# Kernel optimization log

Measured on AMD Instinct MI355X. Metric: run time of the kernel, lower is better.

The kernel has to match this reference:

```python
import jax, jax.numpy as jnp
import numpy as np

B, S, D, H = 8, 256, 16, 256
NH, DH, L = 8, H // 8, 3
H2, H4, FF = H // 2, H // 4, 2 * H


def _ln(x, g, b, eps=1e-5):
    m = jnp.mean(x, axis=-1, keepdims=True)
    v = jnp.var(x, axis=-1, keepdims=True)
    return (x - m) / jnp.sqrt(v + eps) * g + b


def setup_inputs() -> dict:
    key = jax.random.key(0)
    ks = iter(jax.random.split(key, 32))
    w = lambda *sh: jax.random.normal(next(ks), sh, jnp.float32) * 0.05
    inp = {
        'parts': jax.random.normal(next(ks), (B, S, D), jnp.float32),
        'target_sequence': jax.random.randint(next(ks), (B, S), 0, S),
        # part encoder
        'W_pe1': w(H2, D), 'b_pe1': jnp.zeros((H2,)),
        'W_pe2': w(H2, H2), 'b_pe2': jnp.zeros((H2,)),
        'pos_emb': w(S, H4),
        # transformer encoder (3 layers, stacked)
        'Wqkv': w(L, 3 * H, H), 'bqkv': jnp.zeros((L, 3 * H)),
        'Wo': w(L, H, H), 'bo': jnp.zeros((L, H)),
        'ln1_g': jnp.ones((L, H)), 'ln1_b': jnp.zeros((L, H)),
        'W1f': w(L, FF, H), 'b1f': jnp.zeros((L, FF)),
        'W2f': w(L, H, FF), 'b2f': jnp.zeros((L, H)),
        'ln2_g': jnp.ones((L, H)), 'ln2_b': jnp.zeros((L, H)),
        # LSTM decoder
        'Wih': w(4 * H, H), 'Whh': w(4 * H, H),
        'bih': jnp.zeros((4 * H,)), 'bhh': jnp.zeros((4 * H,)),
        # pointer
        'Wp': w(H, H), 'bp': jnp.zeros((H,)), 'v_ptr': w(H),
    }
    return inp


def reference(parts, target_sequence, W_pe1, b_pe1, W_pe2, b_pe2, pos_emb,
              Wqkv, bqkv, Wo, bo, ln1_g, ln1_b, W1f, b1f, W2f, b2f, ln2_g, ln2_b,
              Wih, Whh, bih, bhh, Wp, bp, v_ptr):
    Bk, Sk = parts.shape[:2]
    # ---- encode_inputs (dropout inactive in eval) ----
    pe = jax.nn.relu(parts @ W_pe1.T + b_pe1) @ W_pe2.T + b_pe2          # [B,S,H/2]
    pos = jnp.broadcast_to(pos_emb[None, :Sk], (Bk, Sk, H4))              # [B,S,H/4]
    pad = jnp.zeros((Bk, Sk, H - H2 - H4), parts.dtype)
    x = jnp.concatenate([pe, pos, pad], axis=-1)                          # [B,S,H]
    scale = 1.0 / np.sqrt(DH)
    for l in range(L):  # post-norm transformer encoder layers
        qkv = x @ Wqkv[l].T + bqkv[l]
        q, k, v = jnp.split(qkv, 3, axis=-1)
        q = q.reshape(Bk, Sk, NH, DH)
        k = k.reshape(Bk, Sk, NH, DH)
        v = v.reshape(Bk, Sk, NH, DH)
        att = jax.nn.softmax(jnp.einsum('bqhd,bkhd->bhqk', q, k) * scale, axis=-1)
        o = jnp.einsum('bhqk,bkhd->bqhd', att, v).reshape(Bk, Sk, H)
        o = o @ Wo[l].T + bo[l]
        x = _ln(x + o, ln1_g[l], ln1_b[l])
        f = jax.nn.relu(x @ W1f[l].T + b1f[l]) @ W2f[l].T + b2f[l]
        x = _ln(x + f, ln2_g[l], ln2_b[l])
    enc = x                                                               # [B,S,H]
    # ---- teacher-forced LSTM decode (teacher_forcing_ratio=1.0) ----
    gathered = jnp.take_along_axis(enc, target_sequence[:, :, None], axis=1)  # [B,T,H]
    dec_in = jnp.concatenate([jnp.zeros((Bk, 1, H), enc.dtype), gathered[:, :-1]], 1)
    dec_in = dec_in.transpose(1, 0, 2)                                    # [T,B,H]

    def step(carry, xt):
        h, c = carry
        g = xt @ Wih.T + bih + h @ Whh.T + bhh
        i, f, gg, o = jnp.split(g, 4, axis=-1)
        c = jax.nn.sigmoid(f) * c + jax.nn.sigmoid(i) * jnp.tanh(gg)
        h = jax.nn.sigmoid(o) * jnp.tanh(c)
        return (h, c), h

    h0 = jnp.zeros((Bk, H), enc.dtype)
    _, dec_out = jax.lax.scan(step, (h0, h0), dec_in)
    dec_out = dec_out.transpose(1, 0, 2)                                  # [B,T,H]
    # ---- pointer logits: v . tanh(Wp d_t + Wp e_i), batched over (t,i) ----
    pd = dec_out @ Wp.T + bp                                              # [B,T,H]
    pen = enc @ Wp.T + bp                                                 # [B,S,H]
    logits = jnp.tanh(pd[:, :, None, :] + pen[:, None, :, :]) @ v_ptr     # [B,T,S]
    return logits
```

## Files before the change

kernel.cpp:

```cpp
#include <hip/hip_runtime.h>
#include <cstdint>
#include <cstddef>

typedef _Float16 h2 __attribute__((ext_vector_type(2)));
typedef short bf16x8 __attribute__((ext_vector_type(8)));
typedef float f32x4 __attribute__((ext_vector_type(4)));

__device__ __forceinline__ float sigf(float x) { return 1.0f / (1.0f + __expf(-x)); }
__device__ __forceinline__ float tanhfast(float x) {
  float e = __expf(-2.0f * fabsf(x));
  float t = (1.0f - e) / (1.0f + e);
  return copysignf(t, x);
}
__device__ __forceinline__ h2 cvt2(float a, float b) {
  h2 r; r.x = (_Float16)a; r.y = (_Float16)b; return r;
}
__device__ __forceinline__ h2 bch2(unsigned int u) { return __builtin_bit_cast(h2, u); }
__device__ __forceinline__ unsigned int bcu(h2 v) { return __builtin_bit_cast(unsigned int, v); }
__device__ __forceinline__ unsigned short f2bf(float f) {
  unsigned int u = __float_as_uint(f);
  u = (u + 0x7fffu + ((u >> 16) & 1u)) >> 16;
  return (unsigned short)u;
}

__device__ __forceinline__ float fdot2f(h2 a, h2 b, float c) {
#if __has_builtin(__builtin_amdgcn_fdot2)
  return __builtin_amdgcn_fdot2(a, b, c, false);
#else
  return fmaf((float)a.x, (float)b.x, fmaf((float)a.y, (float)b.y, c));
#endif
}

__global__ void convert_bf(const float* __restrict__ src, ushort* __restrict__ dst, int n) {
  int i = blockIdx.x * 256 + threadIdx.x;
  if (i < n) dst[i] = f2bf(src[i]);
}

__global__ void part_encoder(const float* __restrict__ parts, const float* __restrict__ Wpe1,
                             const float* __restrict__ bpe1, const float* __restrict__ Wpe2,
                             const float* __restrict__ bpe2, const float* __restrict__ pos,
                             float* __restrict__ x, ushort* __restrict__ xb) {
  __shared__ float prow[16];
  __shared__ float pe1[128];
  int row = blockIdx.x;
  int s = row & 255;
  int tid = threadIdx.x;
  if (tid < 16) prow[tid] = parts[row * 16 + tid];
  __syncthreads();
  float a = bpe1[tid];
#pragma unroll
  for (int k = 0; k < 16; ++k) a = fmaf(prow[k], Wpe1[tid * 16 + k], a);
  pe1[tid] = fmaxf(a, 0.0f);
  __syncthreads();
  float a2 = bpe2[tid];
  for (int k = 0; k < 128; ++k) a2 = fmaf(pe1[k], Wpe2[tid * 128 + k], a2);
  x[(size_t)row * 256 + tid] = a2;
  xb[(size_t)row * 256 + tid] = f2bf(a2);
  if (tid < 64) {
    float p = pos[s * 64 + tid];
    x[(size_t)row * 256 + 128 + tid] = p;
    xb[(size_t)row * 256 + 128 + tid] = f2bf(p);
    x[(size_t)row * 256 + 192 + tid] = 0.0f;
    xb[(size_t)row * 256 + 192 + tid] = 0;
  }
}

template <int ACT, int OUTBF>
__global__ __launch_bounds__(256) void gemm_bf16(
    const ushort* __restrict__ A, const ushort* __restrict__ Wt,
    const float* __restrict__ bias1, const float* __restrict__ bias2,
    void* __restrict__ Cout, int N, int K) {
  int wid = threadIdx.x >> 6;
  int lane = threadIdx.x & 63;
  int m0 = blockIdx.y * 64 + wid * 16;
  int n0 = blockIdx.x * 64;
  int r15 = lane & 15;
  int kg = lane >> 4;
  f32x4 acc0 = {0.f, 0.f, 0.f, 0.f}, acc1 = acc0, acc2 = acc0, acc3 = acc0;
  const ushort* arow = A + (size_t)(m0 + r15) * K + kg * 8;
  const ushort* w0 = Wt + (size_t)(n0 + r15) * K + kg * 8;
  const ushort* w1 = w0 + (size_t)16 * K;
  const ushort* w2 = w0 + (size_t)32 * K;
  const ushort* w3 = w0 + (size_t)48 * K;
  for (int k0 = 0; k0 < K; k0 += 32) {
    bf16x8 af = *(const bf16x8*)(arow + k0);
    bf16x8 b0 = *(const bf16x8*)(w0 + k0);
    bf16x8 b1 = *(const bf16x8*)(w1 + k0);
    bf16x8 b2 = *(const bf16x8*)(w2 + k0);
    bf16x8 b3 = *(const bf16x8*)(w3 + k0);
    acc0 = __builtin_amdgcn_mfma_f32_16x16x32_bf16(af, b0, acc0, 0, 0, 0);
    acc1 = __builtin_amdgcn_mfma_f32_16x16x32_bf16(af, b1, acc1, 0, 0, 0);
    acc2 = __builtin_amdgcn_mfma_f32_16x16x32_bf16(af, b2, acc2, 0, 0, 0);
    acc3 = __builtin_amdgcn_mfma_f32_16x16x32_bf16(af, b3, acc3, 0, 0, 0);
  }
#pragma unroll
  for (int nn = 0; nn < 4; ++nn) {
    f32x4 a = (nn == 0) ? acc0 : (nn == 1) ? acc1 : (nn == 2) ? acc2 : acc3;
    int n = n0 + nn * 16 + r15;
    float bsum = bias1[n] + (bias2 ? bias2[n] : 0.0f);
#pragma unroll
    for (int r = 0; r < 4; ++r) {
      int m = m0 + kg * 4 + r;
      float v = a[r] + bsum;
      if (ACT == 1) v = fmaxf(v, 0.0f);
      if (OUTBF == 1)
        ((ushort*)Cout)[(size_t)m * N + n] = f2bf(v);
      else
        ((float*)Cout)[(size_t)m * N + n] = v;
    }
  }
}

__global__ void attn_kernel(const float* __restrict__ qkv, ushort* __restrict__ attout) {
  extern __shared__ float sm[];
  float* kl = sm;
  float* ql = sm + 256 * 33;
  float* sc = sm + 256 * 33 + 32 * 33;
  int qt = blockIdx.x, h = blockIdx.y, b = blockIdx.z;
  int tid = threadIdx.x;
  {
    int j = tid;
    const float* src = qkv + (size_t)(b * 256 + j) * 768 + 256 + h * 32;
#pragma unroll
    for (int d = 0; d < 32; d += 4) {
      float4 v = *(const float4*)(src + d);
      kl[j * 33 + d] = v.x; kl[j * 33 + d + 1] = v.y; kl[j * 33 + d + 2] = v.z; kl[j * 33 + d + 3] = v.w;
    }
  }
  {
    int i = tid >> 3, d4 = (tid & 7) * 4;
    const float* src = qkv + (size_t)(b * 256 + qt * 32 + i) * 768 + h * 32;
    float4 v = *(const float4*)(src + d4);
    ql[i * 33 + d4] = v.x; ql[i * 33 + d4 + 1] = v.y; ql[i * 33 + d4 + 2] = v.z; ql[i * 33 + d4 + 3] = v.w;
  }
  __syncthreads();
  int i = tid >> 3, c = tid & 7;
  const float scale = 0.17677669529663687f;
  float sv[32];
  float mx = -1e30f;
  for (int jj = 0; jj < 32; ++jj) {
    int j = jj * 8 + c;
    float s = 0.0f;
#pragma unroll
    for (int d = 0; d < 32; ++d) s = fmaf(ql[i * 33 + d], kl[j * 33 + d], s);
    s *= scale;
    sv[jj] = s;
    mx = fmaxf(mx, s);
  }
  mx = fmaxf(mx, __shfl_xor(mx, 1));
  mx = fmaxf(mx, __shfl_xor(mx, 2));
  mx = fmaxf(mx, __shfl_xor(mx, 4));
  float sum = 0.0f;
  for (int jj = 0; jj < 32; ++jj) {
    float p = __expf(sv[jj] - mx);
    sc[i * 257 + jj * 8 + c] = p;
    sum += p;
  }
  sum += __shfl_xor(sum, 1);
  sum += __shfl_xor(sum, 2);
  sum += __shfl_xor(sum, 4);
  float inv = 1.0f / sum;
  __syncthreads();
  float a0 = 0, a1 = 0, a2 = 0, a3 = 0;
  int d0 = c * 4;
  const float* vbase = qkv + 512 + h * 32 + d0;
  for (int j = 0; j < 256; ++j) {
    float p = sc[i * 257 + j];
    float4 v = *(const float4*)(vbase + (size_t)(b * 256 + j) * 768);
    a0 = fmaf(p, v.x, a0); a1 = fmaf(p, v.y, a1); a2 = fmaf(p, v.z, a2); a3 = fmaf(p, v.w, a3);
  }
  int orow = b * 256 + qt * 32 + i;
  ushort4 o4;
  o4.x = f2bf(a0 * inv); o4.y = f2bf(a1 * inv); o4.z = f2bf(a2 * inv); o4.w = f2bf(a3 * inv);
  *(ushort4*)&attout[(size_t)orow * 256 + h * 32 + d0] = o4;
}

__global__ void ln_residual(float* __restrict__ x, const float* __restrict__ o,
                            const float* __restrict__ g, const float* __restrict__ bt,
                            ushort* __restrict__ xb) {
  int row = blockIdx.x, tid = threadIdx.x;
  float e = x[(size_t)row * 256 + tid] + o[(size_t)row * 256 + tid];
  float s = e, q = e * e;
#pragma unroll
  for (int off = 32; off >= 1; off >>= 1) {
    s += __shfl_xor(s, off);
    q += __shfl_xor(q, off);
  }
  __shared__ float ps[4], pq[4];
  int wid = tid >> 6, lane = tid & 63;
  if (lane == 0) { ps[wid] = s; pq[wid] = q; }
  __syncthreads();
  float St = ps[0] + ps[1] + ps[2] + ps[3];
  float Qt = pq[0] + pq[1] + pq[2] + pq[3];
  float mean = St * (1.0f / 256.0f);
  float var = Qt * (1.0f / 256.0f) - mean * mean;
  float y = (e - mean) * rsqrtf(var + 1e-5f) * g[tid] + bt[tid];
  x[(size_t)row * 256 + tid] = y;
  xb[(size_t)row * 256 + tid] = f2bf(y);
}

__global__ void gather_dec_in(const ushort* __restrict__ encb, const int* __restrict__ ts,
                              ushort* __restrict__ dec_in) {
  int bx = blockIdx.x;
  int t = bx >> 3, b = bx & 7;
  int tid = threadIdx.x;
  ushort4 v = {0, 0, 0, 0};
  if (t > 0) {
    int sidx = ts[b * 256 + t - 1];
    v = *(const ushort4*)&encb[((size_t)(b * 256 + sidx)) * 256 + tid * 4];
  }
  *(ushort4*)&dec_in[(size_t)bx * 256 + tid * 4] = v;
}

__global__ __attribute__((amdgpu_flat_work_group_size(512, 512), amdgpu_waves_per_eu(1, 1)))
void lstm_scan(const float* __restrict__ Xw, const float* __restrict__ Whh,
               ushort* __restrict__ dec_out) {
  extern __shared__ char smem[];
  uint4* wlds = (uint4*)smem;
  h2* hbuf = (h2*)(smem + 131072);
  int b = blockIdx.x;
  int t0 = threadIdx.x;
  int u = t0 >> 1, p = t0 & 1;
  int rA = u + 256 * p;
  int rB = u + 512 + 256 * p;

  h2 w0[96], w1[96];
  {
    const float4* sA = (const float4*)(Whh + (size_t)rA * 256);
    const float4* sB = (const float4*)(Whh + (size_t)rB * 256);
#pragma unroll
    for (int k = 0; k < 48; ++k) {
      float4 v = sA[k];
      w0[2 * k] = cvt2(v.x, v.y);
      w0[2 * k + 1] = cvt2(v.z, v.w);
    }
#pragma unroll
    for (int k = 0; k < 48; ++k) {
      float4 v = sB[k];
      w1[2 * k] = cvt2(v.x, v.y);
      w1[2 * k + 1] = cvt2(v.z, v.w);
    }
#pragma unroll
    for (int qc = 0; qc < 8; ++qc) {
      float4 vA0 = sA[48 + 2 * qc], vA1 = sA[48 + 2 * qc + 1];
      float4 vB0 = sB[48 + 2 * qc], vB1 = sB[48 + 2 * qc + 1];
      uint4 uA, uB;
      uA.x = bcu(cvt2(vA0.x, vA0.y)); uA.y = bcu(cvt2(vA0.z, vA0.w));
      uA.z = bcu(cvt2(vA1.x, vA1.y)); uA.w = bcu(cvt2(vA1.z, vA1.w));
      uB.x = bcu(cvt2(vB0.x, vB0.y)); uB.y = bcu(cvt2(vB0.z, vB0.w));
      uB.z = bcu(cvt2(vB1.x, vB1.y)); uB.w = bcu(cvt2(vB1.z, vB1.w));
      wlds[qc * 1024 + rA] = uA;
      wlds[qc * 1024 + rB] = uB;
    }
  }
  if (t0 < 128) ((uint4*)hbuf)[t0 & 63] = make_uint4(0, 0, 0, 0);
  float c = 0.0f;
  float xnA = Xw[(size_t)b * 1024 + rA];
  float xnB = Xw[(size_t)b * 1024 + rB];
  __syncthreads();

  for (int t = 0; t < 256; ++t) {
    float xwA = xnA, xwB = xnB;
    if (t < 255) {
      const float* xp = Xw + (size_t)((t + 1) * 8 + b) * 1024;
      xnA = xp[rA]; xnB = xp[rB];
    }
    const uint4* hb = (const uint4*)(hbuf + (size_t)(t & 1) * 128);
    float a0 = 0.0f, a1 = 0.0f;
#pragma unroll
    for (int q = 0; q < 24; ++q) {
      uint4 hv = hb[q];
      h2 hx = bch2(hv.x), hy = bch2(hv.y), hz = bch2(hv.z), hw = bch2(hv.w);
      a0 = fdot2f(w0[4 * q], hx, a0); a0 = fdot2f(w0[4 * q + 1], hy, a0);
      a0 = fdot2f(w0[4 * q + 2], hz, a0); a0 = fdot2f(w0[4 * q + 3], hw, a0);
      a1 = fdot2f(w1[4 * q], hx, a1); a1 = fdot2f(w1[4 * q + 1], hy, a1);
      a1 = fdot2f(w1[4 * q + 2], hz, a1); a1 = fdot2f(w1[4 * q + 3], hw, a1);
    }
#pragma unroll
    for (int qc = 0; qc < 8; ++qc) {
      uint4 hv = hb[24 + qc];
      h2 hx = bch2(hv.x), hy = bch2(hv.y), hz = bch2(hv.z), hw = bch2(hv.w);
      uint4 uA = wlds[qc * 1024 + rA];
      uint4 uB = wlds[qc * 1024 + rB];
      a0 = fdot2f(bch2(uA.x), hx, a0); a0 = fdot2f(bch2(uA.y), hy, a0);
      a0 = fdot2f(bch2(uA.z), hz, a0); a0 = fdot2f(bch2(uA.w), hw, a0);
      a1 = fdot2f(bch2(uB.x), hx, a1); a1 = fdot2f(bch2(uB.y), hy, a1);
      a1 = fdot2f(bch2(uB.z), hz, a1); a1 = fdot2f(bch2(uB.w), hw, a1);
    }
    a0 += xwA;
    a1 += xwB;
    float ev = sigf(a0) * tanhfast(a1);
    float ep = __shfl_xor(ev, 1);
    if (p == 1) {
      c = sigf(a0) * c + ep;
      float hv_ = sigf(a1) * tanhfast(c);
      ((_Float16*)(hbuf + (size_t)((t + 1) & 1) * 128))[u] = (_Float16)hv_;
      dec_out[((size_t)(b * 256 + t)) * 256 + u] = f2bf(hv_);
    }
    __syncthreads();
  }
}

__global__ void transpose_pen(const float* __restrict__ pen, float* __restrict__ penT) {
  int bx = blockIdx.x;
  int b = bx >> 8, h = bx & 255;
  int i = threadIdx.x;
  penT[(size_t)bx * 256 + i] = pen[((size_t)(b * 256 + i)) * 256 + h];
}

__global__ void pointer_kernel(const float* __restrict__ pd, const float* __restrict__ penT,
                               const float* __restrict__ vptr, float* __restrict__ out) {
  __shared__ float pdr[256];
  __shared__ float vl[256];
  int bx = blockIdx.x;
  int b = bx >> 8;
  int tid = threadIdx.x;
  pdr[tid] = pd[(size_t)bx * 256 + tid];
  vl[tid] = vptr[tid];
  __syncthreads();
  const float* pT = penT + (size_t)b * 256 * 256;
  float acc = 0.0f;
  for (int h = 0; h < 256; ++h) {
    acc = fmaf(vl[h], tanhfast(pdr[h] + pT[(size_t)h * 256 + tid]), acc);
  }
  out[(size_t)bx * 256 + tid] = acc;
}

extern "C" void kernel_launch(void* const* d_in, const int* in_sizes, int n_in,
                              void* d_out, int out_size, void* d_ws, size_t ws_size,
                              hipStream_t stream) {
  const float* parts = (const float*)d_in[0];
  const int* ts = (const int*)d_in[1];
  const float* Wpe1 = (const float*)d_in[2];
  const float* bpe1 = (const float*)d_in[3];
  const float* Wpe2 = (const float*)d_in[4];
  const float* bpe2 = (const float*)d_in[5];
  const float* pos = (const float*)d_in[6];
  const float* Wqkv = (const float*)d_in[7];
  const float* bqkv = (const float*)d_in[8];
  const float* Wo = (const float*)d_in[9];
  const float* bo = (const float*)d_in[10];
  const float* ln1g = (const float*)d_in[11];
  const float* ln1b = (const float*)d_in[12];
  const float* W1f = (const float*)d_in[13];
  const float* b1f = (const float*)d_in[14];
  const float* W2f = (const float*)d_in[15];
  const float* b2f = (const float*)d_in[16];
  const float* ln2g = (const float*)d_in[17];
  const float* ln2b = (const float*)d_in[18];
  const float* Wih = (const float*)d_in[19];
  const float* Whh = (const float*)d_in[20];
  const float* bih = (const float*)d_in[21];
  const float* bhh = (const float*)d_in[22];
  const float* Wp = (const float*)d_in[23];
  const float* bp = (const float*)d_in[24];
  const float* vptr = (const float*)d_in[25];
  float* out = (float*)d_out;

  float* W = (float*)d_ws;
  float* xbuf = W;
  ushort* xbf = (ushort*)(W + 524288);
  float* SCR = W + 786432;
  float* qkvb = SCR;
  float* obuf = SCR + 1572864;
  float* Xw = SCR;
  float* pdb = SCR;
  float* penb = SCR + 524288;
  float* penTb = SCR + 1048576;
  ushort* attbf = (ushort*)(W + 2883584);
  ushort* ffbf = (ushort*)(W + 3145728);
  ushort* dec_inbf = (ushort*)(W + 3145728);
  ushort* dec_outbf = (ushort*)(W + 3407872);
  ushort* wqkvbf = (ushort*)(W + 3670016);
  ushort* wobf   = (ushort*)(W + 3964928);
  ushort* w1fbf  = (ushort*)(W + 4063232);
  ushort* w2fbf  = (ushort*)(W + 4259840);
  ushort* wihbf  = (ushort*)(W + 4456448);
  ushort* wpbf   = (ushort*)(W + 4587520);

  const int attnLDS = (256 * 33 + 32 * 33 + 32 * 257) * 4;
  const int scanLDS = 131072 + 1024;
  hipFuncSetAttribute((const void*)attn_kernel, hipFuncAttributeMaxDynamicSharedMemorySize, attnLDS);
  hipFuncSetAttribute((const void*)lstm_scan, hipFuncAttributeMaxDynamicSharedMemorySize, scanLDS);

  convert_bf<<<(589824 + 255) / 256, 256, 0, stream>>>(Wqkv, wqkvbf, 589824);
  convert_bf<<<(196608 + 255) / 256, 256, 0, stream>>>(Wo, wobf, 196608);
  convert_bf<<<(393216 + 255) / 256, 256, 0, stream>>>(W1f, w1fbf, 393216);
  convert_bf<<<(393216 + 255) / 256, 256, 0, stream>>>(W2f, w2fbf, 393216);
  convert_bf<<<(262144 + 255) / 256, 256, 0, stream>>>(Wih, wihbf, 262144);
  convert_bf<<<(65536 + 255) / 256, 256, 0, stream>>>(Wp, wpbf, 65536);

  part_encoder<<<2048, 128, 0, stream>>>(parts, Wpe1, bpe1, Wpe2, bpe2, pos, xbuf, xbf);
  for (int l = 0; l < 3; ++l) {
    gemm_bf16<0, 0><<<dim3(12, 32), 256, 0, stream>>>(xbf, wqkvbf + (size_t)l * 196608,
                                                      bqkv + l * 768, nullptr, qkvb, 768, 256);
    attn_kernel<<<dim3(8, 8, 8), 256, attnLDS, stream>>>(qkvb, attbf);
    gemm_bf16<0, 0><<<dim3(4, 32), 256, 0, stream>>>(attbf, wobf + (size_t)l * 65536,
                                                     bo + l * 256, nullptr, obuf, 256, 256);
    ln_residual<<<2048, 256, 0, stream>>>(xbuf, obuf, ln1g + l * 256, ln1b + l * 256, xbf);
    gemm_bf16<1, 1><<<dim3(8, 32), 256, 0, stream>>>(xbf, w1fbf + (size_t)l * 131072,
                                                     b1f + l * 512, nullptr, ffbf, 512, 256);
    gemm_bf16<0, 0><<<dim3(4, 32), 256, 0, stream>>>(ffbf, w2fbf + (size_t)l * 131072,
                                                     b2f + l * 256, nullptr, obuf, 256, 512);
    ln_residual<<<2048, 256, 0, stream>>>(xbuf, obuf, ln2g + l * 256, ln2b + l * 256, xbf);
  }
  gather_dec_in<<<2048, 64, 0, stream>>>(xbf, ts, dec_inbf);
  gemm_bf16<0, 0><<<dim3(16, 32), 256, 0, stream>>>(dec_inbf, wihbf, bih, bhh, Xw, 1024, 256);
  lstm_scan<<<8, 512, scanLDS, stream>>>(Xw, Whh, dec_outbf);
  gemm_bf16<0, 0><<<dim3(4, 32), 256, 0, stream>>>(dec_outbf, wpbf, bp, nullptr, pdb, 256, 256);
  gemm_bf16<0, 0><<<dim3(4, 32), 256, 0, stream>>>(xbf, wpbf, bp, nullptr, penb, 256, 256);
  transpose_pen<<<2048, 256, 0, stream>>>(penb, penTb);
  pointer_kernel<<<2048, 256, 0, stream>>>(pdb, penTb, vptr, out);
}
```

Measured before the change: 863.2 us.

## Quantize LSTM recurrence to int8 sdot4, merge weight conversions, fuse pen transpose

After: 849.1 us. About the same (-1.6%).

```diff
diff --git a/kernel.cpp b/kernel.cpp
--- a/kernel.cpp
+++ b/kernel.cpp
@@ -5,6 +5,12 @@
 typedef _Float16 h2 __attribute__((ext_vector_type(2)));
 typedef short bf16x8 __attribute__((ext_vector_type(8)));
 typedef float f32x4 __attribute__((ext_vector_type(4)));
+
+#if __has_builtin(__builtin_amdgcn_sdot4)
+#define HAVE_SDOT4 1
+#else
+#define HAVE_SDOT4 0
+#endif
 
 __device__ __forceinline__ float sigf(float x) { return 1.0f / (1.0f + __expf(-x)); }
 __device__ __forceinline__ float tanhfast(float x) {
@@ -31,9 +37,24 @@
 #endif
 }
 
-__global__ void convert_bf(const float* __restrict__ src, ushort* __restrict__ dst, int n) {
+__global__ void convert_all(const float* __restrict__ s0, ushort* __restrict__ d0,
+                            const float* __restrict__ s1, ushort* __restrict__ d1,
+                            const float* __restrict__ s2, ushort* __restrict__ d2,
+                            const float* __restrict__ s3, ushort* __restrict__ d3,
+                            const float* __restrict__ s4, ushort* __restrict__ d4,
+                            const float* __restrict__ s5, ushort* __restrict__ d5) {
   int i = blockIdx.x * 256 + threadIdx.x;
-  if (i < n) dst[i] = f2bf(src[i]);
+  if (i < 589824) { d0[i] = f2bf(s0[i]); return; }
+  i -= 589824;
+  if (i < 196608) { d1[i] = f2bf(s1[i]); return; }
+  i -= 196608;
+  if (i < 393216) { d2[i] = f2bf(s2[i]); return; }
+  i -= 393216;
+  if (i < 393216) { d3[i] = f2bf(s3[i]); return; }
+  i -= 393216;
+  if (i < 262144) { d4[i] = f2bf(s4[i]); return; }
+  i -= 262144;
+  if (i < 65536) d5[i] = f2bf(s5[i]);
 }
 
 __global__ void part_encoder(const float* __restrict__ parts, const float* __restrict__ Wpe1,
@@ -65,7 +86,7 @@
   }
 }
 
-template <int ACT, int OUTBF>
+template <int ACT, int OUT>
 __global__ __launch_bounds__(256) void gemm_bf16(
     const ushort* __restrict__ A, const ushort* __restrict__ Wt,
     const float* __restrict__ bias1, const float* __restrict__ bias2,
@@ -98,15 +119,22 @@
     f32x4 a = (nn == 0) ? acc0 : (nn == 1) ? acc1 : (nn == 2) ? acc2 : acc3;
     int n = n0 + nn * 16 + r15;
     float bsum = bias1[n] + (bias2 ? bias2[n] : 0.0f);
-#pragma unroll
-    for (int r = 0; r < 4; ++r) {
-      int m = m0 + kg * 4 + r;
-      float v = a[r] + bsum;
-      if (ACT == 1) v = fmaxf(v, 0.0f);
-      if (OUTBF == 1)
-        ((ushort*)Cout)[(size_t)m * N + n] = f2bf(v);
-      else
-        ((float*)Cout)[(size_t)m * N + n] = v;
+    if (OUT == 3) {
+      int b = m0 >> 8;
+      int mloc = (m0 & 255) + kg * 4;
+      float4 o4 = {a[0] + bsum, a[1] + bsum, a[2] + bsum, a[3] + bsum};
+      *(float4*)&((float*)Cout)[((size_t)(b * 256 + n)) * 256 + mloc] = o4;
+    } else {
+#pragma unroll
+      for (int r = 0; r < 4; ++r) {
+        int m = m0 + kg * 4 + r;
+        float v = a[r] + bsum;
+        if (ACT == 1) v = fmaxf(v, 0.0f);
+        if (OUT == 1)
+          ((ushort*)Cout)[(size_t)m * N + n] = f2bf(v);
+        else
+          ((float*)Cout)[(size_t)m * N + n] = v;
+      }
     }
   }
 }
@@ -212,9 +240,114 @@
   *(ushort4*)&dec_in[(size_t)bx * 256 + tid * 4] = v;
 }
 
+__global__ __attribute__((amdgpu_flat_work_group_size(512, 512)))
+void lstm_scan_i8(const float* __restrict__ Xw, const float* __restrict__ Whh,
+                  ushort* __restrict__ dec_out) {
+#if HAVE_SDOT4
+  extern __shared__ char smem[];
+  unsigned int* w8l = (unsigned int*)smem;
+  unsigned int* h8 = (unsigned int*)(smem + 81920);
+  const uint4* w8v = (const uint4*)smem;
+  int b = blockIdx.x;
+  int t0 = threadIdx.x;
+  int u = t0 >> 1, p = t0 & 1;
+  int rA = u + 256 * p;
+  int rB = u + 512 + 256 * p;
+
+  unsigned int wA[44], wB[44];
+  float srA, srB;
+#define QROW(WARR, SR, R)                                                      \
+  {                                                                            \
+    const float4* s4_ = (const float4*)(Whh + (size_t)(R) * 256);              \
+    float mx_ = 1e-20f;                                                        \
+    for (int j = 0; j < 64; ++j) {                                             \
+      float4 v = s4_[j];                                                       \
+      mx_ = fmaxf(mx_, fmaxf(fmaxf(fabsf(v.x), fabsf(v.y)),                    \
+                             fmaxf(fabsf(v.z), fabsf(v.w))));                  \
+    }                                                                          \
+    float inv_ = 127.0f / mx_;                                                 \
+    SR = mx_ * (1.0f / 16129.0f);                                              \
+    _Pragma("unroll") for (int j = 0; j < 64; ++j) {                           \
+      float4 v = s4_[j];                                                       \
+      unsigned int b0_ = (unsigned int)((int)rintf(v.x * inv_)) & 255u;        \
+      unsigned int b1_ = (unsigned int)((int)rintf(v.y * inv_)) & 255u;        \
+      unsigned int b2_ = (unsigned int)((int)rintf(v.z * inv_)) & 255u;        \
+      unsigned int b3_ = (unsigned int)((int)rintf(v.w * inv_)) & 255u;        \
+      unsigned int word_ = b0_ | (b1_ << 8) | (b2_ << 16) | (b3_ << 24);       \
+      if (j < 44) WARR[j] = word_;                                             \
+      else {                                                                   \
+        int jj_ = j - 44;                                                      \
+        w8l[(jj_ >> 2) * 4096 + (R) * 4 + (jj_ & 3)] = word_;                  \
+      }                                                                        \
+    }                                                                          \
+  }
+  QROW(wA, srA, rA)
+  QROW(wB, srB, rB)
+#undef QROW
+  if (t0 < 128) h8[t0] = 0u;
+  float c = 0.0f;
+  float xnA = Xw[(size_t)b * 1024 + rA];
+  float xnB = Xw[(size_t)b * 1024 + rB];
+  __syncthreads();
+
+  for (int t = 0; t < 256; ++t) {
+    float xwA = xnA, xwB = xnB;
+    if (t < 255) {
+      const float* xp = Xw + (size_t)((t + 1) * 8 + b) * 1024;
+      xnA = xp[rA]; xnB = xp[rB];
+    }
+    const uint4* hq = (const uint4*)(h8 + (t & 1) * 64);
+    int aA0 = 0, aA1 = 0, aA2 = 0, aA3 = 0;
+    int aB0 = 0, aB1 = 0, aB2 = 0, aB3 = 0;
+#pragma unroll
+    for (int jg = 0; jg < 11; ++jg) {
+      uint4 h4 = hq[jg];
+      aA0 = __builtin_amdgcn_sdot4(wA[4 * jg + 0], h4.x, aA0, false);
+      aA1 = __builtin_amdgcn_sdot4(wA[4 * jg + 1], h4.y, aA1, false);
+      aA2 = __builtin_amdgcn_sdot4(wA[4 * jg + 2], h4.z, aA2, false);
+      aA3 = __builtin_amdgcn_sdot4(wA[4 * jg + 3], h4.w, aA3, false);
+      aB0 = __builtin_amdgcn_sdot4(wB[4 * jg + 0], h4.x, aB0, false);
+      aB1 = __builtin_amdgcn_sdot4(wB[4 * jg + 1], h4.y, aB1, false);
+      aB2 = __builtin_amdgcn_sdot4(wB[4 * jg + 2], h4.z, aB2, false);
+      aB3 = __builtin_amdgcn_sdot4(wB[4 * jg + 3], h4.w, aB3, false);
+    }
+#pragma unroll
+    for (int g = 0; g < 5; ++g) {
+      uint4 h4 = hq[11 + g];
+      uint4 a4 = w8v[g * 1024 + rA];
+      uint4 b4 = w8v[g * 1024 + rB];
+      aA0 = __builtin_amdgcn_sdot4(a4.x, h4.x, aA0, false);
+      aA1 = __builtin_amdgcn_sdot4(a4.y, h4.y, aA1, false);
+      aA2 = __builtin_amdgcn_sdot4(a4.z, h4.z, aA2, false);
+      aA3 = __builtin_amdgcn_sdot4(a4.w, h4.w, aA3, false);
+      aB0 = __builtin_amdgcn_sdot4(b4.x, h4.x, aB0, false);
+      aB1 = __builtin_amdgcn_sdot4(b4.y, h4.y, aB1, false);
+      aB2 = __builtin_amdgcn_sdot4(b4.z, h4.z, aB2, false);
+      aB3 = __builtin_amdgcn_sdot4(b4.w, h4.w, aB3, false);
+    }
+    float gA = (float)((aA0 + aA1) + (aA2 + aA3)) * srA + xwA;
+    float gB = (float)((aB0 + aB1) + (aB2 + aB3)) * srB + xwB;
+    float ev = sigf(gA) * tanhfast(gB);
+    float ep = __shfl_xor(ev, 1);
+    float cn = sigf(gA) * c + ep;
+    float hv_ = sigf(gB) * tanhfast(cn);
+    if (p == 1) {
+      c = cn;
+      dec_out[((size_t)(b * 256 + t)) * 256 + u] = f2bf(hv_);
+    }
+    int iv = (int)rintf(hv_ * 127.0f);
+    unsigned int word = ((unsigned int)iv & 255u) << (8 * (u & 3));
+    word |= (unsigned int)__shfl_xor((int)word, 2);
+    word |= (unsigned int)__shfl_xor((int)word, 4);
+    if (p == 1 && (u & 3) == 0) h8[((t + 1) & 1) * 64 + (u >> 2)] = word;
+    __syncthreads();
+  }
+#endif
+}
+
 __global__ __attribute__((amdgpu_flat_work_group_size(512, 512), amdgpu_waves_per_eu(1, 1)))
-void lstm_scan(const float* __restrict__ Xw, const float* __restrict__ Whh,
-               ushort* __restrict__ dec_out) {
+void lstm_scan512(const float* __restrict__ Xw, const float* __restrict__ Whh,
+                  ushort* __restrict__ dec_out) {
   extern __shared__ char smem[];
   uint4* wlds = (uint4*)smem;
   h2* hbuf = (h2*)(smem + 131072);
@@ -299,13 +432,6 @@
     }
     __syncthreads();
   }
-}
-
-__global__ void transpose_pen(const float* __restrict__ pen, float* __restrict__ penT) {
-  int bx = blockIdx.x;
-  int b = bx >> 8, h = bx & 255;
-  int i = threadIdx.x;
-  penT[(size_t)bx * 256 + i] = pen[((size_t)(b * 256 + i)) * 256 + h];
 }
 
 __global__ void pointer_kernel(const float* __restrict__ pd, const float* __restrict__ penT,
@@ -365,7 +491,6 @@
   float* obuf = SCR + 1572864;
   float* Xw = SCR;
   float* pdb = SCR;
-  float* penb = SCR + 524288;
   float* penTb = SCR + 1048576;
   ushort* attbf = (ushort*)(W + 2883584);
   ushort* ffbf = (ushort*)(W + 3145728);
@@ -379,16 +504,17 @@
   ushort* wpbf   = (ushort*)(W + 4587520);
 
   const int attnLDS = (256 * 33 + 32 * 33 + 32 * 257) * 4;
-  const int scanLDS = 131072 + 1024;
+  const int scan512LDS = 131072 + 1024;
+  const int scanI8LDS = 81920 + 512;
   hipFuncSetAttribute((const void*)attn_kernel, hipFuncAttributeMaxDynamicSharedMemorySize, attnLDS);
-  hipFuncSetAttribute((const void*)lstm_scan, hipFuncAttributeMaxDynamicSharedMemorySize, scanLDS);
-
-  convert_bf<<<(589824 + 255) / 256, 256, 0, stream>>>(Wqkv, wqkvbf, 589824);
-  convert_bf<<<(196608 + 255) / 256, 256, 0, stream>>>(Wo, wobf, 196608);
-  convert_bf<<<(393216 + 255) / 256, 256, 0, stream>>>(W1f, w1fbf, 393216);
-  convert_bf<<<(393216 + 255) / 256, 256, 0, stream>>>(W2f, w2fbf, 393216);
-  convert_bf<<<(262144 + 255) / 256, 256, 0, stream>>>(Wih, wihbf, 262144);
-  convert_bf<<<(65536 + 255) / 256, 256, 0, stream>>>(Wp, wpbf, 65536);
+#if HAVE_SDOT4
+  hipFuncSetAttribute((const void*)lstm_scan_i8, hipFuncAttributeMaxDynamicSharedMemorySize, scanI8LDS);
+#else
+  hipFuncSetAttribute((const void*)lstm_scan512, hipFuncAttributeMaxDynamicSharedMemorySize, scan512LDS);
+#endif
+
+  convert_all<<<7424, 256, 0, stream>>>(Wqkv, wqkvbf, Wo, wobf, W1f, w1fbf,
+                                        W2f, w2fbf, Wih, wihbf, Wp, wpbf);
 
   part_encoder<<<2048, 128, 0, stream>>>(parts, Wpe1, bpe1, Wpe2, bpe2, pos, xbuf, xbf);
   for (int l = 0; l < 3; ++l) {
@@ -406,9 +532,12 @@
   }
   gather_dec_in<<<2048, 64, 0, stream>>>(xbf, ts, dec_inbf);
   gemm_bf16<0, 0><<<dim3(16, 32), 256, 0, stream>>>(dec_inbf, wihbf, bih, bhh, Xw, 1024, 256);
-  lstm_scan<<<8, 512, scanLDS, stream>>>(Xw, Whh, dec_outbf);
+#if HAVE_SDOT4
+  lstm_scan_i8<<<8, 512, scanI8LDS, stream>>>(Xw, Whh, dec_outbf);
+#else
+  lstm_scan512<<<8, 512, scan512LDS, stream>>>(Xw, Whh, dec_outbf);
+#endif
   gemm_bf16<0, 0><<<dim3(4, 32), 256, 0, stream>>>(dec_outbf, wpbf, bp, nullptr, pdb, 256, 256);
-  gemm_bf16<0, 0><<<dim3(4, 32), 256, 0, stream>>>(xbf, wpbf, bp, nullptr, penb, 256, 256);
-  transpose_pen<<<2048, 256, 0, stream>>>(penb, penTb);
+  gemm_bf16<0, 3><<<dim3(4, 32), 256, 0, stream>>>(xbf, wpbf, bp, nullptr, penTb, 256, 256);
   pointer_kernel<<<2048, 256, 0, stream>>>(pdb, penTb, vptr, out);
 }
```

## Run LSTM recurrence with FP8 MFMA, fuse weight conversions and pen transpose

Applied to the files above, without the earlier changes.

Measured after the change: 848.5 us. Within noise of the previous version (-1.7%).

```diff
diff --git a/kernel.cpp b/kernel.cpp
--- a/kernel.cpp
+++ b/kernel.cpp
@@ -5,6 +5,12 @@
 typedef _Float16 h2 __attribute__((ext_vector_type(2)));
 typedef short bf16x8 __attribute__((ext_vector_type(8)));
 typedef float f32x4 __attribute__((ext_vector_type(4)));
+
+#if __has_builtin(__builtin_amdgcn_mfma_f32_16x16x32_fp8_fp8)
+#define HAVE_FP8MFMA 1
+#else
+#define HAVE_FP8MFMA 0
+#endif
 
 __device__ __forceinline__ float sigf(float x) { return 1.0f / (1.0f + __expf(-x)); }
 __device__ __forceinline__ float tanhfast(float x) {
@@ -31,9 +37,54 @@
 #endif
 }
 
-__global__ void convert_bf(const float* __restrict__ src, ushort* __restrict__ dst, int n) {
+__device__ __forceinline__ unsigned int f2fp8(float x) {
+  unsigned int s = (__float_as_uint(x) & 0x80000000u) >> 24;
+  float ax = fabsf(x);
+  if (!(ax >= 0.015625f)) return s;
+  if (ax > 448.0f) ax = 448.0f;
+  unsigned int u = __float_as_uint(ax);
+  u += 0x7FFFFu + ((u >> 20) & 1u);
+  int e4 = (int)(u >> 23) - 120;
+  unsigned int m3 = (u >> 20) & 7u;
+  if (e4 > 15) { e4 = 15; m3 = 6u; }
+  return s | ((unsigned int)e4 << 3) | m3;
+}
+
+__global__ void convert_all(const float* __restrict__ s0, ushort* __restrict__ d0,
+                            const float* __restrict__ s1, ushort* __restrict__ d1,
+                            const float* __restrict__ s2, ushort* __restrict__ d2,
+                            const float* __restrict__ s3, ushort* __restrict__ d3,
+                            const float* __restrict__ s4, ushort* __restrict__ d4,
+                            const float* __restrict__ s5, ushort* __restrict__ d5) {
   int i = blockIdx.x * 256 + threadIdx.x;
-  if (i < n) dst[i] = f2bf(src[i]);
+  if (i < 589824) { d0[i] = f2bf(s0[i]); return; }
+  i -= 589824;
+  if (i < 196608) { d1[i] = f2bf(s1[i]); return; }
+  i -= 196608;
+  if (i < 393216) { d2[i] = f2bf(s2[i]); return; }
+  i -= 393216;
+  if (i < 393216) { d3[i] = f2bf(s3[i]); return; }
+  i -= 393216;
+  if (i < 262144) { d4[i] = f2bf(s4[i]); return; }
+  i -= 262144;
+  if (i < 65536) d5[i] = f2bf(s5[i]);
+}
+
+__global__ void quant_whh(const float* __restrict__ Whh, unsigned char* __restrict__ W8,
+                          float* __restrict__ rsc) {
+  __shared__ float wmx[4];
+  int row = blockIdx.x, tid = threadIdx.x;
+  float v = Whh[(size_t)row * 256 + tid];
+  float mx = fabsf(v);
+#pragma unroll
+  for (int off = 32; off >= 1; off >>= 1) mx = fmaxf(mx, __shfl_xor(mx, off));
+  if ((tid & 63) == 0) wmx[tid >> 6] = mx;
+  __syncthreads();
+  float rowmax = fmaxf(fmaxf(wmx[0], wmx[1]), fmaxf(wmx[2], wmx[3]));
+  rowmax = fmaxf(rowmax, 1e-8f);
+  float scale = 240.0f / rowmax;
+  W8[(size_t)row * 256 + tid] = (unsigned char)f2fp8(v * scale);
+  if (tid == 0) rsc[row] = rowmax * (1.0f / 57600.0f);
 }
 
 __global__ void part_encoder(const float* __restrict__ parts, const float* __restrict__ Wpe1,
@@ -65,7 +116,7 @@
   }
 }
 
-template <int ACT, int OUTBF>
+template <int ACT, int OUT>
 __global__ __launch_bounds__(256) void gemm_bf16(
     const ushort* __restrict__ A, const ushort* __restrict__ Wt,
     const float* __restrict__ bias1, const float* __restrict__ bias2,
@@ -98,15 +149,22 @@
     f32x4 a = (nn == 0) ? acc0 : (nn == 1) ? acc1 : (nn == 2) ? acc2 : acc3;
     int n = n0 + nn * 16 + r15;
     float bsum = bias1[n] + (bias2 ? bias2[n] : 0.0f);
-#pragma unroll
-    for (int r = 0; r < 4; ++r) {
-      int m = m0 + kg * 4 + r;
-      float v = a[r] + bsum;
-      if (ACT == 1) v = fmaxf(v, 0.0f);
-      if (OUTBF == 1)
-        ((ushort*)Cout)[(size_t)m * N + n] = f2bf(v);
-      else
-        ((float*)Cout)[(size_t)m * N + n] = v;
+    if (OUT == 3) {
+      int b = m0 >> 8;
+      int mloc = (m0 & 255) + kg * 4;
+      float4 o4 = {a[0] + bsum, a[1] + bsum, a[2] + bsum, a[3] + bsum};
+      *(float4*)&((float*)Cout)[((size_t)(b * 256 + n)) * 256 + mloc] = o4;
+    } else {
+#pragma unroll
+      for (int r = 0; r < 4; ++r) {
+        int m = m0 + kg * 4 + r;
+        float v = a[r] + bsum;
+        if (ACT == 1) v = fmaxf(v, 0.0f);
+        if (OUT == 1)
+          ((ushort*)Cout)[(size_t)m * N + n] = f2bf(v);
+        else
+          ((float*)Cout)[(size_t)m * N + n] = v;
+      }
     }
   }
 }
@@ -212,9 +270,130 @@
   *(ushort4*)&dec_in[(size_t)bx * 256 + tid * 4] = v;
 }
 
+__global__ __attribute__((amdgpu_flat_work_group_size(512, 512)))
+void lstm_scan_fp8(const float* __restrict__ Xw, const unsigned char* __restrict__ W8,
+                   const float* __restrict__ rsc, ushort* __restrict__ dec_out) {
+#if HAVE_FP8MFMA
+  extern __shared__ char smem[];
+  uint4* ldsB = (uint4*)smem;
+  uint4* h8v = (uint4*)(smem + 131072);
+  unsigned char* h8b = (unsigned char*)(smem + 131072);
+  float* gl = (float*)(smem + 131584);
+  int b = blockIdx.x;
+  int t0 = threadIdx.x;
+  int w = t0 >> 6, l = t0 & 63;
+  int oct = l >> 4, c15 = l & 15;
+
+  long brg[32];
+#pragma unroll
+  for (int tt = 0; tt < 4; ++tt) {
+    int col = w * 128 + tt * 16 + c15;
+#pragma unroll
+    for (int ks = 0; ks < 8; ++ks)
+      brg[tt * 8 + ks] = *(const long*)(W8 + (size_t)col * 256 + ks * 32 + oct * 8);
+  }
+  for (int tt = 4; tt < 8; ++tt) {
+    int col = w * 128 + tt * 16 + c15;
+    int wt = w * 4 + (tt - 4);
+#pragma unroll
+    for (int kp = 0; kp < 4; ++kp) {
+      const unsigned int* p0 = (const unsigned int*)(W8 + (size_t)col * 256 + (2 * kp) * 32 + oct * 8);
+      const unsigned int* p1 = (const unsigned int*)(W8 + (size_t)col * 256 + (2 * kp + 1) * 32 + oct * 8);
+      uint4 q;
+      q.x = p0[0]; q.y = p0[1]; q.z = p1[0]; q.w = p1[1];
+      ldsB[wt * 256 + kp * 64 + l] = q;
+    }
+  }
+  if (t0 < 32) h8v[t0] = make_uint4(0, 0, 0, 0);
+
+  float c = 0.0f;
+  float rs0 = 0, rs1 = 0, rs2 = 0, rs3 = 0;
+  float xni = 0, xnf = 0, xng = 0, xno = 0;
+  int u = t0;
+  if (t0 < 256) {
+    rs0 = rsc[u]; rs1 = rsc[256 + u]; rs2 = rsc[512 + u]; rs3 = rsc[768 + u];
+    const float* xp = Xw + (size_t)b * 1024;
+    xni = xp[u]; xnf = xp[256 + u]; xng = xp[512 + u]; xno = xp[768 + u];
+  }
+  int hoff = ((u & 31) >> 3) * 64 + ((u >> 5) & 7) * 8 + (u & 7);
+  __syncthreads();
+
+  int cur = 0;
+  for (int t = 0; t < 256; ++t) {
+    float xwi = xni, xwf = xnf, xwg = xng, xwo = xno;
+    if (t0 < 256 && t < 255) {
+      const float* xp = Xw + (size_t)((t + 1) * 8 + b) * 1024;
+      xni = xp[u]; xnf = xp[256 + u]; xng = xp[512 + u]; xno = xp[768 + u];
+    }
+    long A0, A1, A2, A3, A4, A5, A6, A7;
+    {
+      uint4 qa = h8v[cur * 16 + oct * 4 + 0];
+      A0 = __builtin_bit_cast(long, make_uint2(qa.x, qa.y));
+      A1 = __builtin_bit_cast(long, make_uint2(qa.z, qa.w));
+      qa = h8v[cur * 16 + oct * 4 + 1];
+      A2 = __builtin_bit_cast(long, make_uint2(qa.x, qa.y));
+      A3 = __builtin_bit_cast(long, make_uint2(qa.z, qa.w));
+      qa = h8v[cur * 16 + oct * 4 + 2];
+      A4 = __builtin_bit_cast(long, make_uint2(qa.x, qa.y));
+      A5 = __builtin_bit_cast(long, make_uint2(qa.z, qa.w));
+      qa = h8v[cur * 16 + oct * 4 + 3];
+      A6 = __builtin_bit_cast(long, make_uint2(qa.x, qa.y));
+      A7 = __builtin_bit_cast(long, make_uint2(qa.z, qa.w));
+    }
+    float gv[8];
+#pragma unroll
+    for (int tt = 0; tt < 4; ++tt) {
+      f32x4 acc = {0.f, 0.f, 0.f, 0.f};
+      acc = __builtin_amdgcn_mfma_f32_16x16x32_fp8_fp8(A0, brg[tt * 8 + 0], acc, 0, 0, 0);
+      acc = __builtin_amdgcn_mfma_f32_16x16x32_fp8_fp8(A1, brg[tt * 8 + 1], acc, 0, 0, 0);
+      acc = __builtin_amdgcn_mfma_f32_16x16x32_fp8_fp8(A2, brg[tt * 8 + 2], acc, 0, 0, 0);
+      acc = __builtin_amdgcn_mfma_f32_16x16x32_fp8_fp8(A3, brg[tt * 8 + 3], acc, 0, 0, 0);
+      acc = __builtin_amdgcn_mfma_f32_16x16x32_fp8_fp8(A4, brg[tt * 8 + 4], acc, 0, 0, 0);
+      acc = __builtin_amdgcn_mfma_f32_16x16x32_fp8_fp8(A5, brg[tt * 8 + 5], acc, 0, 0, 0);
+      acc = __builtin_amdgcn_mfma_f32_16x16x32_fp8_fp8(A6, brg[tt * 8 + 6], acc, 0, 0, 0);
+      acc = __builtin_amdgcn_mfma_f32_16x16x32_fp8_fp8(A7, brg[tt * 8 + 7], acc, 0, 0, 0);
+      gv[tt] = acc[0];
+    }
+#pragma unroll
+    for (int tt = 4; tt < 8; ++tt) {
+      int wt = w * 4 + (tt - 4);
+      f32x4 acc = {0.f, 0.f, 0.f, 0.f};
+#pragma unroll
+      for (int kp = 0; kp < 4; ++kp) {
+        uint4 q = ldsB[wt * 256 + kp * 64 + l];
+        long b0 = __builtin_bit_cast(long, make_uint2(q.x, q.y));
+        long b1 = __builtin_bit_cast(long, make_uint2(q.z, q.w));
+        long Ae = (kp == 0) ? A0 : (kp == 1) ? A2 : (kp == 2) ? A4 : A6;
+        long Ao = (kp == 0) ? A1 : (kp == 1) ? A3 : (kp == 2) ? A5 : A7;
+        acc = __builtin_amdgcn_mfma_f32_16x16x32_fp8_fp8(Ae, b0, acc, 0, 0, 0);
+        acc = __builtin_amdgcn_mfma_f32_16x16x32_fp8_fp8(Ao, b1, acc, 0, 0, 0);
+      }
+      gv[tt] = acc[0];
+    }
+    if (l < 16) {
+#pragma unroll
+      for (int tt = 0; tt < 8; ++tt) gl[w * 128 + tt * 16 + l] = gv[tt];
+    }
+    __syncthreads();
+    if (t0 < 256) {
+      float gi = gl[u] * rs0 + xwi;
+      float gf = gl[256 + u] * rs1 + xwf;
+      float gg = gl[512 + u] * rs2 + xwg;
+      float go = gl[768 + u] * rs3 + xwo;
+      c = sigf(gf) * c + sigf(gi) * tanhfast(gg);
+      float hv_ = sigf(go) * tanhfast(c);
+      dec_out[((size_t)(b * 256 + t)) * 256 + u] = f2bf(hv_);
+      h8b[(cur ^ 1) * 256 + hoff] = (unsigned char)f2fp8(hv_ * 240.0f);
+    }
+    __syncthreads();
+    cur ^= 1;
+  }
+#endif
+}
+
 __global__ __attribute__((amdgpu_flat_work_group_size(512, 512), amdgpu_waves_per_eu(1, 1)))
-void lstm_scan(const float* __restrict__ Xw, const float* __restrict__ Whh,
-               ushort* __restrict__ dec_out) {
+void lstm_scan512(const float* __restrict__ Xw, const float* __restrict__ Whh,
+                  ushort* __restrict__ dec_out) {
   extern __shared__ char smem[];
   uint4* wlds = (uint4*)smem;
   h2* hbuf = (h2*)(smem + 131072);
@@ -299,13 +478,6 @@
     }
     __syncthreads();
   }
-}
-
-__global__ void transpose_pen(const float* __restrict__ pen, float* __restrict__ penT) {
-  int bx = blockIdx.x;
-  int b = bx >> 8, h = bx & 255;
-  int i = threadIdx.x;
-  penT[(size_t)bx * 256 + i] = pen[((size_t)(b * 256 + i)) * 256 + h];
 }
 
 __global__ void pointer_kernel(const float* __restrict__ pd, const float* __restrict__ penT,
@@ -365,7 +537,6 @@
   float* obuf = SCR + 1572864;
   float* Xw = SCR;
   float* pdb = SCR;
-  float* penb = SCR + 524288;
   float* penTb = SCR + 1048576;
   ushort* attbf = (ushort*)(W + 2883584);
   ushort* ffbf = (ushort*)(W + 3145728);
@@ -377,18 +548,24 @@
   ushort* w2fbf  = (ushort*)(W + 4259840);
   ushort* wihbf  = (ushort*)(W + 4456448);
   ushort* wpbf   = (ushort*)(W + 4587520);
+  unsigned char* whh8 = (unsigned char*)(W + 4620288);
+  float* rscb = W + 4685824;
 
   const int attnLDS = (256 * 33 + 32 * 33 + 32 * 257) * 4;
-  const int scanLDS = 131072 + 1024;
+  const int scan512LDS = 131072 + 1024;
+  const int scanFp8LDS = 131072 + 512 + 4096;
   hipFuncSetAttribute((const void*)attn_kernel, hipFuncAttributeMaxDynamicSharedMemorySize, attnLDS);
-  hipFuncSetAttribute((const void*)lstm_scan, hipFuncAttributeMaxDynamicSharedMemorySize, scanLDS);
-
-  convert_bf<<<(589824 + 255) / 256, 256, 0, stream>>>(Wqkv, wqkvbf, 589824);
-  convert_bf<<<(196608 + 255) / 256, 256, 0, stream>>>(Wo, wobf, 196608);
-  convert_bf<<<(393216 + 255) / 256, 256, 0, stream>>>(W1f, w1fbf, 393216);
-  convert_bf<<<(393216 + 255) / 256, 256, 0, stream>>>(W2f, w2fbf, 393216);
-  convert_bf<<<(262144 + 255) / 256, 256, 0, stream>>>(Wih, wihbf, 262144);
-  convert_bf<<<(65536 + 255) / 256, 256, 0, stream>>>(Wp, wpbf, 65536);
+#if HAVE_FP8MFMA
+  hipFuncSetAttribute((const void*)lstm_scan_fp8, hipFuncAttributeMaxDynamicSharedMemorySize, scanFp8LDS);
+#else
+  hipFuncSetAttribute((const void*)lstm_scan512, hipFuncAttributeMaxDynamicSharedMemorySize, scan512LDS);
+#endif
+
+  convert_all<<<7424, 256, 0, stream>>>(Wqkv, wqkvbf, Wo, wobf, W1f, w1fbf,
+                                        W2f, w2fbf, Wih, wihbf, Wp, wpbf);
+#if HAVE_FP8MFMA
+  quant_whh<<<1024, 256, 0, stream>>>(Whh, whh8, rscb);
+#endif
 
   part_encoder<<<2048, 128, 0, stream>>>(parts, Wpe1, bpe1, Wpe2, bpe2, pos, xbuf, xbf);
   for (int l = 0; l < 3; ++l) {
@@ -406,9 +583,12 @@
   }
   gather_dec_in<<<2048, 64, 0, stream>>>(xbf, ts, dec_inbf);
   gemm_bf16<0, 0><<<dim3(16, 32), 256, 0, stream>>>(dec_inbf, wihbf, bih, bhh, Xw, 1024, 256);
-  lstm_scan<<<8, 512, scanLDS, stream>>>(Xw, Whh, dec_outbf);
+#if HAVE_FP8MFMA
+  lstm_scan_fp8<<<8, 512, scanFp8LDS, stream>>>(Xw, whh8, rscb, dec_outbf);
+#else
+  lstm_scan512<<<8, 512, scan512LDS, stream>>>(Xw, Whh, dec_outbf);
+#endif
   gemm_bf16<0, 0><<<dim3(4, 32), 256, 0, stream>>>(dec_outbf, wpbf, bp, nullptr, pdb, 256, 256);
-  gemm_bf16<0, 0><<<dim3(4, 32), 256, 0, stream>>>(xbf, wpbf, bp, nullptr, penb, 256, 256);
-  transpose_pen<<<2048, 256, 0, stream>>>(penb, penTb);
+  gemm_bf16<0, 3><<<dim3(4, 32), 256, 0, stream>>>(xbf, wpbf, bp, nullptr, penTb, 256, 256);
   pointer_kernel<<<2048, 256, 0, stream>>>(pdb, penTb, vptr, out);
 }
```
